# Performance work log

Measured on AMD Instinct MI355X. Metric: run time of the kernel, lower is better.

## Reference

```python
import jax, jax.numpy as jnp
import numpy as np

H = 512
L = 4
A = 16
EPS = 1e-5


def setup_inputs() -> dict:
    key = jax.random.key(0)
    ks = jax.random.split(key, 16)
    B, S = 64, 256
    scale = 0.02
    inp = {
        "hidden": jnp.zeros((B, H), jnp.float32),
        "x": jax.random.normal(ks[0], (B, S, H), jnp.float32),
        "dones": jax.random.randint(ks[1], (B, S), 0, 2).astype(bool),
        "avail_actions": jax.random.randint(ks[2], (B, S, A), 0, 2).astype(bool),
        # MLP stack: L layers of Linear(H,H) + LayerNorm
        "Wl": jax.random.normal(ks[3], (L, H, H), jnp.float32) * scale,
        "bl": jnp.zeros((L, H), jnp.float32),
        "ln_g": jnp.ones((L, H), jnp.float32),
        "ln_b": jnp.zeros((L, H), jnp.float32),
        # GRUCell(H, H): torch layout weight_ih [3H, H] (r, z, n order)
        "W_ih": jax.random.normal(ks[4], (3 * H, H), jnp.float32) * scale,
        "W_hh": jax.random.normal(ks[5], (3 * H, H), jnp.float32) * scale,
        "b_ih": jnp.zeros((3 * H,), jnp.float32),
        "b_hh": jnp.zeros((3 * H,), jnp.float32),
        # output head
        "Wq": jax.random.normal(ks[6], (A, H), jnp.float32) * scale,
        "bq": jnp.zeros((A,), jnp.float32),
    }
    return inp


def _layer_norm(x, g, b):
    mu = jnp.mean(x, axis=-1, keepdims=True)
    var = jnp.mean(jnp.square(x - mu), axis=-1, keepdims=True)
    return (x - mu) * jax.lax.rsqrt(var + EPS) * g + b


def _gru_scan(h0, x, dones, W_ih, W_hh, b_ih, b_hh):
    # Precompute input projections for all timesteps: [B, S, 3H]
    gi = jnp.einsum("bsh,gh->bsg", x, W_ih) + b_ih
    gi_t = jnp.swapaxes(gi, 0, 1)          # [S, B, 3H]
    dones_t = jnp.swapaxes(dones, 0, 1)    # [S, B]

    def step(h, inputs):
        gi_s, done_s = inputs
        h = jnp.where(done_s[:, None], 0.0, h)  # reset carry where done
        gh = h @ W_hh.T + b_hh
        i_r, i_z, i_n = jnp.split(gi_s, 3, axis=-1)
        h_r, h_z, h_n = jnp.split(gh, 3, axis=-1)
        r = jax.nn.sigmoid(i_r + h_r)
        z = jax.nn.sigmoid(i_z + h_z)
        n = jnp.tanh(i_n + r * h_n)
        h_new = (1.0 - z) * n + z * h
        return h_new, h_new

    h_final, outs = jax.lax.scan(step, h0, (gi_t, dones_t))
    return h_final, jnp.swapaxes(outs, 0, 1)  # [B, S, H]


def reference(hidden, x, dones, avail_actions, Wl, bl, ln_g, ln_b,
              W_ih, W_hh, b_ih, b_hh, Wq, bq):
    h = x
    for l in range(L):
        h = jnp.einsum("bsh,oh->bso", h, Wl[l]) + bl[l]
        h = jax.nn.relu(_layer_norm(h, ln_g[l], ln_b[l]))
    hidden_out, rnn_out = _gru_scan(hidden, h, dones, W_ih, W_hh, b_ih, b_hh)
    q = jnp.einsum("bsh,ah->bsa", rnn_out, Wq) + bq
    unavail = 1.0 - avail_actions.astype(q.dtype)
    q = q - unavail * 1e10
    return hidden_out, q
```

## Files before the change

kernel.cpp:

```cpp
#include <hip/hip_runtime.h>
#include <hip/hip_bf16.h>

typedef short short8 __attribute__((ext_vector_type(8)));
typedef float f32x4 __attribute__((ext_vector_type(4)));

#define H 512
#define BATCH 64
#define SEQ 256
#define NROWS 16384
#define NDOM 16
#define HSTCAP 12288

__device__ __forceinline__ float bf2f(unsigned short u) {
    union { unsigned int i; float f; } v;
    v.i = ((unsigned int)u) << 16;
    return v.f;
}
__device__ __forceinline__ unsigned short f2bf(float f) {
    union { float f; unsigned int i; } v;
    v.f = f;
    unsigned int lsb = (v.i >> 16) & 1u;
    v.i += 0x7fffu + lsb;
    return (unsigned short)(v.i >> 16);
}
__device__ __forceinline__ float sigm(float x) { return 1.f / (1.f + __expf(-x)); }
__device__ __forceinline__ float tanh_fast(float x) { return 2.f / (1.f + __expf(-2.f * x)) - 1.f; }

__global__ __launch_bounds__(256) void cvt_init(
    const float* __restrict__ Wl, const float* __restrict__ Wih,
    unsigned short* __restrict__ wlb, unsigned short* __restrict__ wihb,
    unsigned int* __restrict__ meta)
{
    long idx4 = (long)blockIdx.x * 256 + threadIdx.x;
    if (idx4 < 20480) meta[idx4] = 0u;
    long i = idx4 * 4;
    const long N1 = 1048576;
    const long N2 = N1 + 786432;
    const float* src; unsigned short* dst; long off;
    if (i < N1)      { src = Wl;  dst = wlb;  off = i; }
    else if (i < N2) { src = Wih; dst = wihb; off = i - N1; }
    else return;
    float4 v = *(const float4*)(src + off);
    ushort4 o;
    o.x = f2bf(v.x); o.y = f2bf(v.y); o.z = f2bf(v.z); o.w = f2bf(v.w);
    *(ushort4*)(dst + off) = o;
}

__global__ __launch_bounds__(256) void seg_build(
    const int* __restrict__ dones, int* __restrict__ lenArr,
    unsigned int* __restrict__ hist)
{
    __shared__ int d[256];
    const int b = blockIdx.x, s = threadIdx.x;
    d[s] = dones[b * 256 + s];
    __syncthreads();
    int len = 0;
    bool start = (s == 0) || (d[s] != 0);
    if (start) {
        len = 1;
        while (s + len < 256 && d[s + len] == 0) len++;
        atomicAdd(&hist[len], 1u);
    }
    lenArr[b * 256 + s] = len;
}

__global__ __launch_bounds__(256) void seg_offsets(
    const unsigned int* __restrict__ hist, int* __restrict__ Marr,
    unsigned int* __restrict__ offs, unsigned int* __restrict__ ssum)
{
    __shared__ unsigned int h[257];
    __shared__ int Msh[257];
    const int t = threadIdx.x;
    h[t] = hist[t];
    if (t == 0) h[256] = hist[256];
    __syncthreads();
    for (int tt = t; tt <= 256; tt += 256) {
        unsigned int m = 0;
        for (int L = tt + 1; L <= 256; ++L) m += h[L];
        Marr[tt] = (int)m;
        offs[tt] = m;
        Msh[tt] = (int)m;
    }
    __syncthreads();
    if (t == 0) {
        unsigned int acc = 0;
        for (int k = 0; k <= 256; ++k) { ssum[k] = acc; acc += (unsigned int)Msh[k]; }
    }
}

__global__ __launch_bounds__(256) void seg_scatter(
    const int* __restrict__ lenArr, unsigned int* __restrict__ offs,
    int* __restrict__ recs)
{
    const int b = blockIdx.x, s = threadIdx.x;
    int len = lenArr[b * 256 + s];
    if (len > 0) {
        unsigned int pos = atomicAdd(&offs[len], 1u);
        recs[pos] = (b << 16) | s;
    }
}

__global__ __launch_bounds__(256) void pmap_build(
    const int* __restrict__ recs, const int* __restrict__ Marr,
    const unsigned int* __restrict__ ssum, const int* __restrict__ lenArr,
    int* __restrict__ pmap)
{
    const int i = blockIdx.x * 256 + threadIdx.x;
    if (i >= Marr[0]) return;
    int rec = recs[i];
    int b = rec >> 16, st = rec & 0xffff;
    int len = lenArr[b * 256 + st];
    for (int t = 0; t < len; ++t) pmap[b * 256 + st + t] = (int)ssum[t] + i;
}

__global__ __launch_bounds__(256) void h_init(
    const int* __restrict__ recs, const int* __restrict__ Marr,
    const int* __restrict__ dones, const float* __restrict__ hidden,
    unsigned short* __restrict__ hst)
{
    const int w = threadIdx.x >> 6, lane = threadIdx.x & 63;
    const int i = blockIdx.x * 4 + w;
    const int nseg = Marr[0];
    const int c0 = lane * 8;
    unsigned short* dst = hst + (long)i * 512 + c0;
    if (i < nseg) {
        int rec = recs[i];
        int b = rec >> 16, st = rec & 0xffff;
        if (st == 0 && dones[b * 256] == 0) {
            float4 va = *(const float4*)(hidden + b * 512 + c0);
            float4 vb = *(const float4*)(hidden + b * 512 + c0 + 4);
            ushort4 o0 = {f2bf(va.x), f2bf(va.y), f2bf(va.z), f2bf(va.w)};
            ushort4 o1 = {f2bf(vb.x), f2bf(vb.y), f2bf(vb.z), f2bf(vb.w)};
            *(ushort4*)dst = o0; *(ushort4*)(dst + 4) = o1;
            return;
        }
    }
    ushort4 z4 = {0, 0, 0, 0};
    *(ushort4*)dst = z4; *(ushort4*)(dst + 4) = z4;
}

__global__ __launch_bounds__(512) void mlp_gi(
    const float* __restrict__ x,
    const unsigned short* __restrict__ wlb,
    const unsigned short* __restrict__ wihb,
    const float* __restrict__ bl,
    const float* __restrict__ lng,
    const float* __restrict__ lnb,
    const float* __restrict__ bih,
    const int* __restrict__ pmap,
    unsigned short* __restrict__ gi)
{
    __shared__ unsigned short ldsAct[64 * 512];
    __shared__ float red[64 * 16];
    const int tid = threadIdx.x;
    const int lane = tid & 63;
    const int w = tid >> 6;
    const long m0 = (long)blockIdx.x * 64;
    const int l15 = lane & 15;
    const int l4 = lane >> 4;

#pragma unroll
    for (int it = 0; it < 8; ++it) {
        int ch = it * 512 + tid;
        int row = ch >> 6;
        int c = ch & 63;
        const float* xp = x + (m0 + row) * 512 + c * 8;
        float4 a = *(const float4*)xp;
        float4 b4 = *(const float4*)(xp + 4);
        short8 v;
        v[0] = (short)f2bf(a.x);  v[1] = (short)f2bf(a.y);
        v[2] = (short)f2bf(a.z);  v[3] = (short)f2bf(a.w);
        v[4] = (short)f2bf(b4.x); v[5] = (short)f2bf(b4.y);
        v[6] = (short)f2bf(b4.z); v[7] = (short)f2bf(b4.w);
        int byteo = (row * 1024 + c * 16) ^ ((row & 7) << 4);
        *(short8*)((char*)ldsAct + byteo) = v;
    }
    int pm[4][4];
#pragma unroll
    for (int i = 0; i < 4; ++i)
#pragma unroll
        for (int r = 0; r < 4; ++r)
            pm[i][r] = pmap[m0 + i * 16 + l4 * 4 + r];
    __syncthreads();

    for (int l = 0; l < 4; ++l) {
        const unsigned short* W = wlb + (long)l * 512 * 512;
        const unsigned short* wr0 = W + (long)(w * 64 + l15) * 512 + l4 * 8;
        f32x4 acc[4][4];
#pragma unroll
        for (int i = 0; i < 4; ++i)
#pragma unroll
            for (int jn = 0; jn < 4; ++jn) acc[i][jn] = (f32x4){0.f, 0.f, 0.f, 0.f};

#pragma unroll
        for (int kk = 0; kk < 16; ++kk) {
            short8 bfr[4];
#pragma unroll
            for (int jn = 0; jn < 4; ++jn)
                bfr[jn] = *(const short8*)(wr0 + (long)jn * 16 * 512 + kk * 32);
            short8 af[4];
#pragma unroll
            for (int i = 0; i < 4; ++i) {
                int row = i * 16 + l15;
                int byteo = (row * 1024 + kk * 64 + l4 * 16) ^ ((row & 7) << 4);
                af[i] = *(const short8*)((const char*)ldsAct + byteo);
            }
#pragma unroll
            for (int i = 0; i < 4; ++i)
#pragma unroll
                for (int jn = 0; jn < 4; ++jn)
                    acc[i][jn] = __builtin_amdgcn_mfma_f32_16x16x32_bf16(af[i], bfr[jn], acc[i][jn], 0, 0, 0);
        }

        float bz[4], gl[4], bb[4];
#pragma unroll
        for (int jn = 0; jn < 4; ++jn) {
            int n = w * 64 + jn * 16 + l15;
            bz[jn] = bl[l * 512 + n]; gl[jn] = lng[l * 512 + n]; bb[jn] = lnb[l * 512 + n];
        }
#pragma unroll
        for (int i = 0; i < 4; ++i)
#pragma unroll
            for (int jn = 0; jn < 4; ++jn)
#pragma unroll
                for (int r = 0; r < 4; ++r) acc[i][jn][r] += bz[jn];

#pragma unroll
        for (int i = 0; i < 4; ++i) {
#pragma unroll
            for (int r = 0; r < 4; ++r) {
                float sv = 0.f, qv = 0.f;
#pragma unroll
                for (int jn = 0; jn < 4; ++jn) {
                    float v = acc[i][jn][r];
                    sv += v; qv += v * v;
                }
                sv += __shfl_xor(sv, 1); qv += __shfl_xor(qv, 1);
                sv += __shfl_xor(sv, 2); qv += __shfl_xor(qv, 2);
                sv += __shfl_xor(sv, 4); qv += __shfl_xor(qv, 4);
                sv += __shfl_xor(sv, 8); qv += __shfl_xor(qv, 8);
                if (l15 == 0) {
                    int row = i * 16 + l4 * 4 + r;
                    red[row * 16 + w * 2] = sv;
                    red[row * 16 + w * 2 + 1] = qv;
                }
            }
        }
        __syncthreads();

#pragma unroll
        for (int i = 0; i < 4; ++i) {
#pragma unroll
            for (int r = 0; r < 4; ++r) {
                int row = i * 16 + l4 * 4 + r;
                float s_tot = 0.f, q_tot = 0.f;
#pragma unroll
                for (int ww = 0; ww < 8; ++ww) {
                    s_tot += red[row * 16 + ww * 2];
                    q_tot += red[row * 16 + ww * 2 + 1];
                }
                float mu = s_tot * (1.f / 512.f);
                float var = q_tot * (1.f / 512.f) - mu * mu;
                float rs = rsqrtf(var + 1e-5f);
#pragma unroll
                for (int jn = 0; jn < 4; ++jn) {
                    int col = w * 64 + jn * 16 + l15;
                    float v = fmaxf(0.f, (acc[i][jn][r] - mu) * rs * gl[jn] + bb[jn]);
                    int byteo = (row * 1024 + col * 2) ^ ((row & 7) << 4);
                    *(unsigned short*)((char*)ldsAct + byteo) = f2bf(v);
                }
            }
        }
        __syncthreads();
    }

    for (int nc = 0; nc < 3; ++nc) {
        const unsigned short* W = wihb + (long)nc * 512 * 512;
        const unsigned short* wr0 = W + (long)(w * 64 + l15) * 512 + l4 * 8;
        f32x4 acc[4][4];
#pragma unroll
        for (int i = 0; i < 4; ++i)
#pragma unroll
            for (int jn = 0; jn < 4; ++jn) acc[i][jn] = (f32x4){0.f, 0.f, 0.f, 0.f};

#pragma unroll
        for (int kk = 0; kk < 16; ++kk) {
            short8 bfr[4];
#pragma unroll
            for (int jn = 0; jn < 4; ++jn)
                bfr[jn] = *(const short8*)(wr0 + (long)jn * 16 * 512 + kk * 32);
            short8 af[4];
#pragma unroll
            for (int i = 0; i < 4; ++i) {
                int row = i * 16 + l15;
                int byteo = (row * 1024 + kk * 64 + l4 * 16) ^ ((row & 7) << 4);
                af[i] = *(const short8*)((const char*)ldsAct + byteo);
            }
#pragma unroll
            for (int i = 0; i < 4; ++i)
#pragma unroll
                for (int jn = 0; jn < 4; ++jn)
                    acc[i][jn] = __builtin_amdgcn_mfma_f32_16x16x32_bf16(af[i], bfr[jn], acc[i][jn], 0, 0, 0);
        }

#pragma unroll
        for (int jn = 0; jn < 4; ++jn) {
            int colg = nc * 512 + w * 64 + jn * 16 + l15;
            float bz = bih[colg];
#pragma unroll
            for (int i = 0; i < 4; ++i)
#pragma unroll
                for (int r = 0; r < 4; ++r)
                    gi[(long)pm[i][r] * 1536 + colg] = f2bf(acc[i][jn][r] + bz);
        }
    }
}

__device__ __forceinline__ void dbar(unsigned int* __restrict__ dm,
                                     int wg, unsigned int epoch)
{
    __syncthreads();
    const int tid = threadIdx.x;
    if (wg == 0) {
        if (tid == 0)
            __hip_atomic_store(&dm[0], epoch + 1u, __ATOMIC_RELAXED,
                               __HIP_MEMORY_SCOPE_AGENT);
        if (tid < 16) {
            while (__hip_atomic_load(&dm[tid * 32], __ATOMIC_RELAXED,
                                     __HIP_MEMORY_SCOPE_AGENT) <= epoch)
                __builtin_amdgcn_s_sleep(1);
        }
        if (tid == 0)
            __hip_atomic_store(&dm[512], epoch + 1u, __ATOMIC_RELAXED,
                               __HIP_MEMORY_SCOPE_AGENT);
    } else {
        if (tid == 0) {
            __hip_atomic_store(&dm[wg * 32], epoch + 1u, __ATOMIC_RELAXED,
                               __HIP_MEMORY_SCOPE_AGENT);
            while (__hip_atomic_load(&dm[512], __ATOMIC_RELAXED,
                                     __HIP_MEMORY_SCOPE_AGENT) <= epoch)
                __builtin_amdgcn_s_sleep(1);
        }
    }
    __syncthreads();
    __builtin_amdgcn_sched_barrier(0);
}

__global__ __launch_bounds__(256, 1) void gru_seg_scan(
    const unsigned short* __restrict__ gi,
    const float* __restrict__ Whh,
    const float* __restrict__ bhh,
    const int* __restrict__ Marr,
    const unsigned int* __restrict__ ssum,
    const int* __restrict__ recs,
    unsigned short* __restrict__ hstA,
    unsigned short* __restrict__ hstB,
    unsigned short* __restrict__ rnn,
    float* __restrict__ hid_out,
    unsigned int* __restrict__ meta)
{
    __shared__ unsigned short ldsW[96 * 512];
    __shared__ int sMarr[257];
    __shared__ unsigned int sssum[257];
    const int tid = threadIdx.x;
    const int lane = tid & 63;
    const int w = tid >> 6;
    const int jg = blockIdx.x >> 4;
    const int dom = blockIdx.x & 15;
    const int j0 = jg * 32;

    for (int e = tid; e < 96 * 512; e += 256) {
        int rrow = e >> 9;
        int col = e & 511;
        int gate = rrow >> 5;
        int jl = rrow & 31;
        float v = Whh[((long)(gate * 512 + j0 + jl)) * 512 + col];
        int byteo = (rrow * 1024 + col * 2) ^ ((rrow & 7) << 4);
        *(unsigned short*)((char*)ldsW + byteo) = f2bf(v);
    }
    for (int e = tid; e < 257; e += 256) { sMarr[e] = Marr[e]; sssum[e] = ssum[e]; }

    const int jl16 = lane & 15;
    float bhr[2], bhz[2], bhn[2];
#pragma unroll
    for (int jj = 0; jj < 2; ++jj) {
        int jc = j0 + jj * 16 + jl16;
        bhr[jj] = bhh[jc]; bhz[jj] = bhh[512 + jc]; bhn[jj] = bhh[1024 + jc];
    }
    const int rbase = w * 16 + (lane >> 4) * 4;
    const int arowl = w * 16 + jl16;
    const int kcol0 = (lane >> 4) * 8;
    unsigned int* dmeta = meta + 1024 * dom;
    __syncthreads();

    int crec[4], nrec[4];
    unsigned short cgr[4][2], cgz[4][2], cgn[4][2];
    unsigned short ngr[4][2], ngz[4][2], ngn[4][2];

    {
        const int Mt0 = sMarr[0];
        const long b0 = (long)sssum[0];
#pragma unroll
        for (int q = 0; q < 4; ++q) {
            int r = dom * 64 + rbase + q;
            if (r < Mt0) {
                crec[q] = recs[r];
#pragma unroll
                for (int jj = 0; jj < 2; ++jj) {
                    const unsigned short* gp = gi + (b0 + r) * 1536 + j0 + jj * 16 + jl16;
                    cgr[q][jj] = gp[0]; cgz[q][jj] = gp[512]; cgn[q][jj] = gp[1024];
                }
            } else crec[q] = -1;
        }
    }

    for (int t = 0; t < 256; ++t) {
        const int Mt = sMarr[t];
        if (Mt == 0) break;
        const int ntiles = (Mt + 63) >> 6;
        if (dom >= ntiles) break;
        const unsigned short* hsrc = (t & 1) ? hstB : hstA;
        unsigned short* hdst = (t & 1) ? hstA : hstB;
        const long base = (long)sssum[t];

        for (int tt = dom; tt < ntiles; tt += NDOM) {
            const int r0 = tt * 64;

            const unsigned short* arowp = hsrc + ((long)(r0 + arowl)) * 512 + kcol0;
            short8 af[16];
#pragma unroll
            for (int kk = 0; kk < 16; ++kk) {
                const unsigned short* ap = arowp + kk * 32;
                asm volatile("global_load_dwordx4 %0, %1, off sc0"
                             : "=v"(af[kk]) : "v"(ap));
            }
            unsigned int hu[4][2];
#pragma unroll
            for (int q = 0; q < 4; ++q)
#pragma unroll
                for (int jj = 0; jj < 2; ++jj) {
                    const unsigned short* hp = hsrc + (long)(r0 + rbase + q) * 512
                                             + j0 + jj * 16 + jl16;
                    asm volatile("global_load_ushort %0, %1, off sc0"
                                 : "=v"(hu[q][jj]) : "v"(hp));
                }
            asm volatile("s_waitcnt vmcnt(0)" ::: "memory");
            __builtin_amdgcn_sched_barrier(0);

            const bool instep = (tt + NDOM < ntiles);
            if (instep) {
#pragma unroll
                for (int q = 0; q < 4; ++q) {
                    int r = (tt + NDOM) * 64 + rbase + q;
                    if (r < Mt) {
                        nrec[q] = recs[r];
#pragma unroll
                        for (int jj = 0; jj < 2; ++jj) {
                            const unsigned short* gp = gi + (base + r) * 1536 + j0 + jj * 16 + jl16;
                            ngr[q][jj] = gp[0]; ngz[q][jj] = gp[512]; ngn[q][jj] = gp[1024];
                        }
                    } else nrec[q] = -1;
                }
            }

            f32x4 acch[3][2];
#pragma unroll
            for (int g = 0; g < 3; ++g)
#pragma unroll
                for (int jj = 0; jj < 2; ++jj) acch[g][jj] = (f32x4){0.f, 0.f, 0.f, 0.f};

#pragma unroll
            for (int kk = 0; kk < 16; ++kk) {
#pragma unroll
                for (int g = 0; g < 3; ++g)
#pragma unroll
                    for (int jj = 0; jj < 2; ++jj) {
                        int rrow = g * 32 + jj * 16 + jl16;
                        int bbyte = (rrow * 1024 + kk * 64 + ((lane >> 4) * 16)) ^ ((rrow & 7) << 4);
                        short8 bfrag = *(const short8*)((const char*)ldsW + bbyte);
                        acch[g][jj] = __builtin_amdgcn_mfma_f32_16x16x32_bf16(af[kk], bfrag, acch[g][jj], 0, 0, 0);
                    }
            }

#pragma unroll
            for (int q = 0; q < 4; ++q) {
                if (crec[q] >= 0) {
                    int r = r0 + rbase + q;
                    int b = crec[q] >> 16, st = crec[q] & 0xffff;
                    int s = st + t;
#pragma unroll
                    for (int jj = 0; jj < 2; ++jj) {
                        int jc = j0 + jj * 16 + jl16;
                        float heff = bf2f((unsigned short)hu[q][jj]);
                        float rgt = sigm(bf2f(cgr[q][jj]) + acch[0][jj][q] + bhr[jj]);
                        float zgt = sigm(bf2f(cgz[q][jj]) + acch[1][jj][q] + bhz[jj]);
                        float ngt = tanh_fast(bf2f(cgn[q][jj]) + rgt * (acch[2][jj][q] + bhn[jj]));
                        float hnew = (1.f - zgt) * ngt + zgt * heff;
                        unsigned short hb16 = f2bf(hnew);
                        hdst[(long)r * 512 + jc] = hb16;
                        rnn[((long)(b * 256 + s)) * 512 + jc] = hb16;
                        if (s == 255) hid_out[b * 512 + jc] = hnew;
                    }
                }
            }
            if (instep) {
#pragma unroll
                for (int q = 0; q < 4; ++q) {
                    crec[q] = nrec[q];
#pragma unroll
                    for (int jj = 0; jj < 2; ++jj) {
                        cgr[q][jj] = ngr[q][jj]; cgz[q][jj] = ngz[q][jj]; cgn[q][jj] = ngn[q][jj];
                    }
                }
            }
        }

        {
            const int Mt1 = sMarr[t + 1];
            if (Mt1 > 0 && dom < ((Mt1 + 63) >> 6)) {
                const long b1 = (long)sssum[t + 1];
#pragma unroll
                for (int q = 0; q < 4; ++q) {
                    int r = dom * 64 + rbase + q;
                    if (r < Mt1) {
                        crec[q] = recs[r];
#pragma unroll
                        for (int jj = 0; jj < 2; ++jj) {
                            const unsigned short* gp = gi + (b1 + r) * 1536 + j0 + jj * 16 + jl16;
                            cgr[q][jj] = gp[0]; cgz[q][jj] = gp[512]; cgn[q][jj] = gp[1024];
                        }
                    } else crec[q] = -1;
                }
            }
        }
        dbar(dmeta, jg, (unsigned int)t);
    }
}

__global__ __launch_bounds__(256) void qhead(
    const unsigned short* __restrict__ rnn, const float* __restrict__ Wq,
    const float* __restrict__ bq, const int* __restrict__ avail,
    float* __restrict__ qout)
{
    const int w = threadIdx.x >> 6;
    const int lane = threadIdx.x & 63;
    const long row = (long)blockIdx.x * 4 + w;
    const int a = lane & 15;
    const int kc = lane >> 4;
    const unsigned short* hr = rnn + row * H + kc * 128;
    const float* wr = Wq + a * H + kc * 128;
    float sum = 0.f;
#pragma unroll
    for (int i = 0; i < 128; i += 8) {
        short8 hv = *(const short8*)(hr + i);
        float4 wa = *(const float4*)(wr + i);
        float4 wb = *(const float4*)(wr + i + 4);
        sum += bf2f((unsigned short)hv[0]) * wa.x;
        sum += bf2f((unsigned short)hv[1]) * wa.y;
        sum += bf2f((unsigned short)hv[2]) * wa.z;
        sum += bf2f((unsigned short)hv[3]) * wa.w;
        sum += bf2f((unsigned short)hv[4]) * wb.x;
        sum += bf2f((unsigned short)hv[5]) * wb.y;
        sum += bf2f((unsigned short)hv[6]) * wb.z;
        sum += bf2f((unsigned short)hv[7]) * wb.w;
    }
    sum += __shfl_xor(sum, 16);
    sum += __shfl_xor(sum, 32);
    if (kc == 0) {
        float qv = sum + bq[a];
        int av = avail[row * 16 + a];
        if (av == 0) qv -= 1e10f;
        qout[row * 16 + a] = qv;
    }
}

extern "C" void kernel_launch(void* const* d_in, const int* in_sizes, int n_in,
                              void* d_out, int out_size, void* d_ws, size_t ws_size,
                              hipStream_t stream)
{
    const float* hidden = (const float*)d_in[0];
    const float* x      = (const float*)d_in[1];
    const int*   dones  = (const int*)d_in[2];
    const int*   avail  = (const int*)d_in[3];
    const float* Wl     = (const float*)d_in[4];
    const float* bl     = (const float*)d_in[5];
    const float* ln_g   = (const float*)d_in[6];
    const float* ln_b   = (const float*)d_in[7];
    const float* W_ih   = (const float*)d_in[8];
    const float* W_hh   = (const float*)d_in[9];
    const float* b_ih   = (const float*)d_in[10];
    const float* b_hh   = (const float*)d_in[11];
    const float* Wq     = (const float*)d_in[12];
    const float* bq     = (const float*)d_in[13];

    char* p = (char*)d_ws;
    unsigned short* gi   = (unsigned short*)p; p += (size_t)NROWS * 1536 * 2;
    unsigned short* rnn  = (unsigned short*)p; p += (size_t)NROWS * H * 2;
    unsigned short* hst0 = (unsigned short*)p; p += (size_t)HSTCAP * H * 2;
    unsigned short* hst1 = (unsigned short*)p; p += (size_t)HSTCAP * H * 2;
    unsigned short* wlb  = (unsigned short*)p; p += (size_t)4 * H * H * 2;
    unsigned short* wihb = (unsigned short*)p; p += (size_t)3 * H * H * 2;
    int* lenArr = (int*)p;          p += (size_t)NROWS * 4;
    int* recs   = (int*)p;          p += (size_t)NROWS * 4;
    int* pmap   = (int*)p;          p += (size_t)NROWS * 4;
    unsigned int* meta = (unsigned int*)p;  p += 20480 * 4;
    unsigned int* hist = meta + 16384;
    unsigned int* offs = meta + 16672;
    int* Marr = (int*)(meta + 16960);
    unsigned int* ssum = meta + 17248;

    cvt_init<<<1792, 256, 0, stream>>>(Wl, W_ih, wlb, wihb, meta);

    seg_build<<<64, 256, 0, stream>>>(dones, lenArr, hist);
    seg_offsets<<<1, 256, 0, stream>>>(hist, Marr, offs, ssum);
    seg_scatter<<<64, 256, 0, stream>>>(lenArr, offs, recs);
    pmap_build<<<64, 256, 0, stream>>>(recs, Marr, ssum, lenArr, pmap);

    h_init<<<HSTCAP / 4, 256, 0, stream>>>(recs, Marr, dones, hidden, hst0);

    mlp_gi<<<256, 512, 0, stream>>>(x, wlb, wihb, bl, ln_g, ln_b, b_ih, pmap, gi);

    gru_seg_scan<<<256, 256, 0, stream>>>(gi, W_hh, b_hh, Marr, ssum, recs,
                                          hst0, hst1, rnn, (float*)d_out, meta);

    qhead<<<4096, 256, 0, stream>>>(rnn, Wq, bq, avail, (float*)d_out + BATCH * H);
}
```

Measured before the change: 606.2 us.

## Retile MLP GEMMs with LDS-staged weights and split the GRU grid barrier

The fused MLP plus input-projection kernel now uses 32-row tiles with 256 threads and 512 blocks. Weight tiles are staged into LDS through global_load_lds instead of being read by each wave straight from global memory. The gi output is written through an LDS transpose, so each permuted row goes out as coalesced 16-byte stores. In the GRU scan, the grid barrier is split: each group posts its arrival before prefetching the next step's gate inputs and only then waits, so the prefetch overlaps the barrier latency. The cost is more __syncthreads per k-step in the GEMM, and less reuse of each weight tile because fewer rows share it.

```diff
diff --git a/kernel.cpp b/kernel.cpp
--- a/kernel.cpp
+++ b/kernel.cpp
@@ -139,7 +139,7 @@
     *(ushort4*)dst = z4; *(ushort4*)(dst + 4) = z4;
 }
 
-__global__ __launch_bounds__(512) void mlp_gi(
+__global__ __launch_bounds__(256) void mlp_gi(
     const float* __restrict__ x,
     const unsigned short* __restrict__ wlb,
     const unsigned short* __restrict__ wihb,
@@ -150,18 +150,19 @@
     const int* __restrict__ pmap,
     unsigned short* __restrict__ gi)
 {
-    __shared__ unsigned short ldsAct[64 * 512];
-    __shared__ float red[64 * 16];
+    __shared__ unsigned short ldsAct[32 * 512];
+    __shared__ unsigned short ldsW[512 * 32];
+    __shared__ float red[32 * 8];
     const int tid = threadIdx.x;
     const int lane = tid & 63;
     const int w = tid >> 6;
-    const long m0 = (long)blockIdx.x * 64;
+    const long m0 = (long)blockIdx.x * 32;
     const int l15 = lane & 15;
     const int l4 = lane >> 4;
 
 #pragma unroll
     for (int it = 0; it < 8; ++it) {
-        int ch = it * 512 + tid;
+        int ch = it * 256 + tid;
         int row = ch >> 6;
         int c = ch & 63;
         const float* xp = x + (m0 + row) * 512 + c * 8;
@@ -175,175 +176,136 @@
         int byteo = (row * 1024 + c * 16) ^ ((row & 7) << 4);
         *(short8*)((char*)ldsAct + byteo) = v;
     }
-    int pm[4][4];
-#pragma unroll
-    for (int i = 0; i < 4; ++i)
-#pragma unroll
-        for (int r = 0; r < 4; ++r)
-            pm[i][r] = pmap[m0 + i * 16 + l4 * 4 + r];
     __syncthreads();
 
-    for (int l = 0; l < 4; ++l) {
-        const unsigned short* W = wlb + (long)l * 512 * 512;
-        const unsigned short* wr0 = W + (long)(w * 64 + l15) * 512 + l4 * 8;
-        f32x4 acc[4][4];
-#pragma unroll
-        for (int i = 0; i < 4; ++i)
-#pragma unroll
-            for (int jn = 0; jn < 4; ++jn) acc[i][jn] = (f32x4){0.f, 0.f, 0.f, 0.f};
-
-#pragma unroll
-        for (int kk = 0; kk < 16; ++kk) {
-            short8 bfr[4];
-#pragma unroll
-            for (int jn = 0; jn < 4; ++jn)
-                bfr[jn] = *(const short8*)(wr0 + (long)jn * 16 * 512 + kk * 32);
-            short8 af[4];
-#pragma unroll
-            for (int i = 0; i < 4; ++i) {
-                int row = i * 16 + l15;
-                int byteo = (row * 1024 + kk * 64 + l4 * 16) ^ ((row & 7) << 4);
+    for (int u = 0; u < 7; ++u) {
+        const unsigned short* W = (u < 4) ? (wlb + (long)u * 262144)
+                                          : (wihb + (long)(u - 4) * 262144);
+        f32x4 acc[2][8];
+#pragma unroll
+        for (int i = 0; i < 2; ++i)
+#pragma unroll
+            for (int jn = 0; jn < 8; ++jn) acc[i][jn] = (f32x4){0.f, 0.f, 0.f, 0.f};
+
+        for (int kt = 0; kt < 16; ++kt) {
+            __syncthreads();
+#pragma unroll
+            for (int i = 0; i < 8; ++i) {
+                int o = (i * 256 + tid) * 16;
+                int row = o >> 6;
+                int ch = (o & 63) >> 4;
+                long gcol = (long)kt * 64 + (long)((ch ^ (row & 3)) << 4);
+                __builtin_amdgcn_global_load_lds(
+                    (const unsigned int*)((const char*)W + (long)row * 1024 + gcol),
+                    (unsigned int*)(ldsW + (i * 256 + w * 64) * 8), 16, 0, 0);
+            }
+            __syncthreads();
+
+            short8 af[2], bfr[8];
+#pragma unroll
+            for (int i = 0; i < 2; ++i) {
+                int arow = i * 16 + l15;
+                int byteo = (arow * 1024 + kt * 64 + l4 * 16) ^ ((arow & 7) << 4);
                 af[i] = *(const short8*)((const char*)ldsAct + byteo);
             }
 #pragma unroll
-            for (int i = 0; i < 4; ++i)
-#pragma unroll
-                for (int jn = 0; jn < 4; ++jn)
+            for (int jn = 0; jn < 8; ++jn) {
+                int wrow = w * 128 + jn * 16 + l15;
+                int byteo = (wrow * 64 + l4 * 16) ^ ((wrow & 3) << 4);
+                bfr[jn] = *(const short8*)((const char*)ldsW + byteo);
+            }
+#pragma unroll
+            for (int i = 0; i < 2; ++i)
+#pragma unroll
+                for (int jn = 0; jn < 8; ++jn)
                     acc[i][jn] = __builtin_amdgcn_mfma_f32_16x16x32_bf16(af[i], bfr[jn], acc[i][jn], 0, 0, 0);
         }
 
-        float bz[4], gl[4], bb[4];
-#pragma unroll
-        for (int jn = 0; jn < 4; ++jn) {
-            int n = w * 64 + jn * 16 + l15;
-            bz[jn] = bl[l * 512 + n]; gl[jn] = lng[l * 512 + n]; bb[jn] = lnb[l * 512 + n];
+        if (u < 4) {
+            float bz[8], gl[8], bb[8];
+#pragma unroll
+            for (int jn = 0; jn < 8; ++jn) {
+                int n = w * 128 + jn * 16 + l15;
+                bz[jn] = bl[u * 512 + n]; gl[jn] = lng[u * 512 + n]; bb[jn] = lnb[u * 512 + n];
+            }
+#pragma unroll
+            for (int i = 0; i < 2; ++i)
+#pragma unroll
+                for (int jn = 0; jn < 8; ++jn)
+#pragma unroll
+                    for (int r = 0; r < 4; ++r) acc[i][jn][r] += bz[jn];
+
+#pragma unroll
+            for (int i = 0; i < 2; ++i) {
+#pragma unroll
+                for (int r = 0; r < 4; ++r) {
+                    float sv = 0.f, qv = 0.f;
+#pragma unroll
+                    for (int jn = 0; jn < 8; ++jn) {
+                        float v = acc[i][jn][r];
+                        sv += v; qv += v * v;
+                    }
+                    sv += __shfl_xor(sv, 1); qv += __shfl_xor(qv, 1);
+                    sv += __shfl_xor(sv, 2); qv += __shfl_xor(qv, 2);
+                    sv += __shfl_xor(sv, 4); qv += __shfl_xor(qv, 4);
+                    sv += __shfl_xor(sv, 8); qv += __shfl_xor(qv, 8);
+                    if (l15 == 0) {
+                        int row = i * 16 + l4 * 4 + r;
+                        red[row * 8 + w * 2] = sv;
+                        red[row * 8 + w * 2 + 1] = qv;
+                    }
+                }
+            }
+            __syncthreads();
+
+#pragma unroll
+            for (int i = 0; i < 2; ++i) {
+#pragma unroll
+                for (int r = 0; r < 4; ++r) {
+                    int row = i * 16 + l4 * 4 + r;
+                    float s_tot = red[row * 8 + 0] + red[row * 8 + 2] + red[row * 8 + 4] + red[row * 8 + 6];
+                    float q_tot = red[row * 8 + 1] + red[row * 8 + 3] + red[row * 8 + 5] + red[row * 8 + 7];
+                    float mu = s_tot * (1.f / 512.f);
+                    float var = q_tot * (1.f / 512.f) - mu * mu;
+                    float rs = rsqrtf(var + 1e-5f);
+#pragma unroll
+                    for (int jn = 0; jn < 8; ++jn) {
+                        int col = w * 128 + jn * 16 + l15;
+                        float v = fmaxf(0.f, (acc[i][jn][r] - mu) * rs * gl[jn] + bb[jn]);
+                        int byteo = (row * 1024 + col * 2) ^ ((row & 7) << 4);
+                        *(unsigned short*)((char*)ldsAct + byteo) = f2bf(v);
+                    }
+                }
+            }
+            __syncthreads();
+        } else {
+            const int nc = u - 4;
+            __syncthreads();
+#pragma unroll
+            for (int jn = 0; jn < 8; ++jn) {
+                int colg = nc * 512 + w * 128 + jn * 16 + l15;
+                float bz = bih[colg];
+#pragma unroll
+                for (int i = 0; i < 2; ++i)
+#pragma unroll
+                    for (int r = 0; r < 4; ++r) {
+                        int row = i * 16 + l4 * 4 + r;
+                        int col = w * 128 + jn * 16 + l15;
+                        int byteo = (row * 1024 + col * 2) ^ ((row & 7) << 4);
+                        *(unsigned short*)((char*)ldsW + byteo) = f2bf(acc[i][jn][r] + bz);
+                    }
+            }
+            __syncthreads();
+#pragma unroll
+            for (int k = 0; k < 8; ++k) {
+                int row = w * 8 + k;
+                int pmr = pmap[m0 + row];
+                int byteo = (row * 1024 + lane * 16) ^ ((row & 7) << 4);
+                short8 v = *(const short8*)((const char*)ldsW + byteo);
+                *(short8*)(gi + (long)pmr * 1536 + nc * 512 + lane * 8) = v;
+            }
         }
-#pragma unroll
-        for (int i = 0; i < 4; ++i)
-#pragma unroll
-            for (int jn = 0; jn < 4; ++jn)
-#pragma unroll
-                for (int r = 0; r < 4; ++r) acc[i][jn][r] += bz[jn];
-
-#pragma unroll
-        for (int i = 0; i < 4; ++i) {
-#pragma unroll
-            for (int r = 0; r < 4; ++r) {
-                float sv = 0.f, qv = 0.f;
-#pragma unroll
-                for (int jn = 0; jn < 4; ++jn) {
-                    float v = acc[i][jn][r];
-                    sv += v; qv += v * v;
-                }
-                sv += __shfl_xor(sv, 1); qv += __shfl_xor(qv, 1);
-                sv += __shfl_xor(sv, 2); qv += __shfl_xor(qv, 2);
-                sv += __shfl_xor(sv, 4); qv += __shfl_xor(qv, 4);
-                sv += __shfl_xor(sv, 8); qv += __shfl_xor(qv, 8);
-                if (l15 == 0) {
-                    int row = i * 16 + l4 * 4 + r;
-                    red[row * 16 + w * 2] = sv;
-                    red[row * 16 + w * 2 + 1] = qv;
-                }
-            }
-        }
-        __syncthreads();
-
-#pragma unroll
-        for (int i = 0; i < 4; ++i) {
-#pragma unroll
-            for (int r = 0; r < 4; ++r) {
-                int row = i * 16 + l4 * 4 + r;
-                float s_tot = 0.f, q_tot = 0.f;
-#pragma unroll
-                for (int ww = 0; ww < 8; ++ww) {
-                    s_tot += red[row * 16 + ww * 2];
-                    q_tot += red[row * 16 + ww * 2 + 1];
-                }
-                float mu = s_tot * (1.f / 512.f);
-                float var = q_tot * (1.f / 512.f) - mu * mu;
-                float rs = rsqrtf(var + 1e-5f);
-#pragma unroll
-                for (int jn = 0; jn < 4; ++jn) {
-                    int col = w * 64 + jn * 16 + l15;
-                    float v = fmaxf(0.f, (acc[i][jn][r] - mu) * rs * gl[jn] + bb[jn]);
-                    int byteo = (row * 1024 + col * 2) ^ ((row & 7) << 4);
-                    *(unsigned short*)((char*)ldsAct + byteo) = f2bf(v);
-                }
-            }
-        }
-        __syncthreads();
-    }
-
-    for (int nc = 0; nc < 3; ++nc) {
-        const unsigned short* W = wihb + (long)nc * 512 * 512;
-        const unsigned short* wr0 = W + (long)(w * 64 + l15) * 512 + l4 * 8;
-        f32x4 acc[4][4];
-#pragma unroll
-        for (int i = 0; i < 4; ++i)
-#pragma unroll
-            for (int jn = 0; jn < 4; ++jn) acc[i][jn] = (f32x4){0.f, 0.f, 0.f, 0.f};
-
-#pragma unroll
-        for (int kk = 0; kk < 16; ++kk) {
-            short8 bfr[4];
-#pragma unroll
-            for (int jn = 0; jn < 4; ++jn)
-                bfr[jn] = *(const short8*)(wr0 + (long)jn * 16 * 512 + kk * 32);
-            short8 af[4];
-#pragma unroll
-            for (int i = 0; i < 4; ++i) {
-                int row = i * 16 + l15;
-                int byteo = (row * 1024 + kk * 64 + l4 * 16) ^ ((row & 7) << 4);
-                af[i] = *(const short8*)((const char*)ldsAct + byteo);
-            }
-#pragma unroll
-            for (int i = 0; i < 4; ++i)
-#pragma unroll
-                for (int jn = 0; jn < 4; ++jn)
-                    acc[i][jn] = __builtin_amdgcn_mfma_f32_16x16x32_bf16(af[i], bfr[jn], acc[i][jn], 0, 0, 0);
-        }
-
-#pragma unroll
-        for (int jn = 0; jn < 4; ++jn) {
-            int colg = nc * 512 + w * 64 + jn * 16 + l15;
-            float bz = bih[colg];
-#pragma unroll
-            for (int i = 0; i < 4; ++i)
-#pragma unroll
-                for (int r = 0; r < 4; ++r)
-                    gi[(long)pm[i][r] * 1536 + colg] = f2bf(acc[i][jn][r] + bz);
-        }
-    }
-}
-
-__device__ __forceinline__ void dbar(unsigned int* __restrict__ dm,
-                                     int wg, unsigned int epoch)
-{
-    __syncthreads();
-    const int tid = threadIdx.x;
-    if (wg == 0) {
-        if (tid == 0)
-            __hip_atomic_store(&dm[0], epoch + 1u, __ATOMIC_RELAXED,
-                               __HIP_MEMORY_SCOPE_AGENT);
-        if (tid < 16) {
-            while (__hip_atomic_load(&dm[tid * 32], __ATOMIC_RELAXED,
-                                     __HIP_MEMORY_SCOPE_AGENT) <= epoch)
-                __builtin_amdgcn_s_sleep(1);
-        }
-        if (tid == 0)
-            __hip_atomic_store(&dm[512], epoch + 1u, __ATOMIC_RELAXED,
-                               __HIP_MEMORY_SCOPE_AGENT);
-    } else {
-        if (tid == 0) {
-            __hip_atomic_store(&dm[wg * 32], epoch + 1u, __ATOMIC_RELAXED,
-                               __HIP_MEMORY_SCOPE_AGENT);
-            while (__hip_atomic_load(&dm[512], __ATOMIC_RELAXED,
-                                     __HIP_MEMORY_SCOPE_AGENT) <= epoch)
-                __builtin_amdgcn_s_sleep(1);
-        }
-    }
-    __syncthreads();
-    __builtin_amdgcn_sched_barrier(0);
+    }
 }
 
 __global__ __launch_bounds__(256, 1) void gru_seg_scan(
@@ -515,6 +477,10 @@
             }
         }
 
+        __syncthreads();
+        if (tid == 0)
+            __hip_atomic_store(&dmeta[jg * 32], (unsigned int)t + 1u,
+                               __ATOMIC_RELAXED, __HIP_MEMORY_SCOPE_AGENT);
         {
             const int Mt1 = sMarr[t + 1];
             if (Mt1 > 0 && dom < ((Mt1 + 63) >> 6)) {
@@ -533,7 +499,25 @@
                 }
             }
         }
-        dbar(dmeta, jg, (unsigned int)t);
+        __builtin_amdgcn_sched_barrier(0);
+        if (jg == 0) {
+            if (tid < 16) {
+                while (__hip_atomic_load(&dmeta[tid * 32], __ATOMIC_RELAXED,
+                                         __HIP_MEMORY_SCOPE_AGENT) <= (unsigned int)t)
+                    __builtin_amdgcn_s_sleep(1);
+            }
+            if (tid == 0)
+                __hip_atomic_store(&dmeta[512], (unsigned int)t + 1u,
+                                   __ATOMIC_RELAXED, __HIP_MEMORY_SCOPE_AGENT);
+        } else {
+            if (tid == 0) {
+                while (__hip_atomic_load(&dmeta[512], __ATOMIC_RELAXED,
+                                         __HIP_MEMORY_SCOPE_AGENT) <= (unsigned int)t)
+                    __builtin_amdgcn_s_sleep(1);
+            }
+        }
+        __syncthreads();
+        __builtin_amdgcn_sched_barrier(0);
     }
 }
 
@@ -618,7 +602,7 @@
 
     h_init<<<HSTCAP / 4, 256, 0, stream>>>(recs, Marr, dones, hidden, hst0);
 
-    mlp_gi<<<256, 512, 0, stream>>>(x, wlb, wihb, bl, ln_g, ln_b, b_ih, pmap, gi);
+    mlp_gi<<<512, 256, 0, stream>>>(x, wlb, wihb, bl, ln_g, ln_b, b_ih, pmap, gi);
 
     gru_seg_scan<<<256, 256, 0, stream>>>(gi, W_hh, b_hh, Marr, ssum, recs,
                                           hst0, hst1, rnn, (float*)d_out, meta);
```

New measurement: 657.8 us. 1.09x slower.
